# Optimization experiments

Hardware: AMD Instinct MI355X
Metric: run time of the kernel (lower is better)

## Reference

```python
import jax, jax.numpy as jnp
import numpy as np

DIM = 1024
HEADS = 16
DIM_HEAD = DIM // HEADS  # 64


def setup_inputs() -> dict:
    key = jax.random.key(0)
    k1, k2, k3 = jax.random.split(key, 3)
    x = jax.random.normal(k1, (4, 2048, DIM), dtype=jnp.float32)
    # Linear weights stored as [in, out] so y = x @ W (torch Linear uses x @ W.T; init is random either way)
    w_qkv = jax.random.normal(k2, (DIM, 3 * DIM), dtype=jnp.float32) * (DIM ** -0.5)
    w_out = jax.random.normal(k3, (DIM, DIM), dtype=jnp.float32) * (DIM ** -0.5)
    return {"x": x, "w_qkv": w_qkv, "w_out": w_out}


def reference(x, w_qkv, w_out):
    b, t, d = x.shape
    h, dh = HEADS, DIM_HEAD
    qkv = x @ w_qkv  # [b, t, 3*h*dh]
    q, k, v = jnp.split(qkv, 3, axis=-1)
    split_heads = lambda a: a.reshape(b, t, h, dh).transpose(0, 2, 1, 3)  # [b,h,t,dh]
    q, k, v = map(split_heads, (q, k, v))
    # NOTE: original scales by full model dim d, not per-head dim
    scale = d ** (-0.5)
    dots = jnp.einsum('bhie,bhje->bhij', q, k) * scale  # [b,h,t,t]
    attn = jax.nn.softmax(dots, axis=-1)
    out = jnp.einsum('bhij,bhje->bhie', attn, v)  # [b,h,t,dh]
    out = out.transpose(0, 2, 1, 3).reshape(b, t, h * dh)
    return out @ w_out
```

## Files before the change

### kernel.cpp

```cpp
#include <hip/hip_runtime.h>


typedef __bf16 bf16x8 __attribute__((ext_vector_type(8)));
typedef __bf16 bf16x4 __attribute__((ext_vector_type(4)));
typedef float f32x4 __attribute__((ext_vector_type(4)));
typedef float f32x2 __attribute__((ext_vector_type(2)));
typedef unsigned short ushort8 __attribute__((ext_vector_type(8)));

#define MFMA16(a, b, c) __builtin_amdgcn_mfma_f32_16x16x32_bf16((a), (b), (c), 0, 0, 0)

__device__ __forceinline__ unsigned short f2bf(float f) {
  unsigned int u = __float_as_uint(f);
  u = (u + 0x7FFFu + ((u >> 16) & 1u)) >> 16;
  return (unsigned short)u;
}

__device__ __forceinline__ float fast_exp2(float x) {
#if __has_builtin(__builtin_amdgcn_exp2f)
  return __builtin_amdgcn_exp2f(x);
#else
  float r;
  asm("v_exp_f32 %0, %1" : "=v"(r) : "v"(x));
  return r;
#endif
}

__device__ __forceinline__ void gload_lds16(const unsigned short* g, unsigned short* l) {
  __builtin_amdgcn_global_load_lds(
      (const __attribute__((address_space(1))) unsigned int*)g,
      (__attribute__((address_space(3))) unsigned int*)l, 16, 0, 0);
}

__global__ __launch_bounds__(256) void prep_kernel(
    const float* __restrict__ x, unsigned short* __restrict__ xb,
    const float* __restrict__ wqkv, unsigned short* __restrict__ WqkvT,
    const float* __restrict__ wout, unsigned short* __restrict__ WoutT) {
  const int bid = blockIdx.x;
  const int tid = threadIdx.x;
  if (bid < 4096) {
    int i = (bid * 256 + tid) * 8;
    float4 a = *(const float4*)&x[i];
    float4 b = *(const float4*)&x[i + 4];
    ushort8 o = {f2bf(a.x), f2bf(a.y), f2bf(a.z), f2bf(a.w),
                 f2bf(b.x), f2bf(b.y), f2bf(b.z), f2bf(b.w)};
    *(ushort8*)&xb[i] = o;
    return;
  }
  __shared__ float t[32][33];
  const float* in;
  unsigned short* out;
  int C, scale_limit, c0, r0;
  if (bid < 4096 + 3072) {
    int tj = bid - 4096;
    in = wqkv; out = WqkvT; C = 3072; scale_limit = 1024;
    c0 = (tj % 96) * 32; r0 = (tj / 96) * 32;
  } else {
    int tj = bid - 7168;
    in = wout; out = WoutT; C = 1024; scale_limit = 0;
    c0 = (tj & 31) * 32; r0 = (tj >> 5) * 32;
  }
  const float kQScale = 0.045084220027780106f;
#pragma unroll
  for (int i = 0; i < 4; ++i) {
    int e = tid + i * 256;
    int r = e >> 5, c = e & 31;
    t[r][c] = in[(size_t)(r0 + r) * C + c0 + c];
  }
  __syncthreads();
#pragma unroll
  for (int i = 0; i < 4; ++i) {
    int e = tid + i * 256;
    int r = e >> 5, c = e & 31;
    float v = t[c][r];
    if (c0 + r < scale_limit) v *= kQScale;
    out[(size_t)(c0 + r) * 1024 + r0 + c] = f2bf(v);
  }
}

template <int MODE>
__global__ __launch_bounds__(256) void gemm_bt(
    const unsigned short* __restrict__ A, const unsigned short* __restrict__ Bt,
    void* __restrict__ Cv, unsigned short* __restrict__ VT,
    int M, int N, int K) {
  __shared__ unsigned short As[128 * 32];
  __shared__ unsigned short Bs[128 * 32];
  const int tid = threadIdx.x;
  const int wave = tid >> 6, lane = tid & 63;
  const int g = lane >> 4, ln = lane & 15;
  const int wm = wave >> 1, wn = wave & 1;
  const long bm = (long)blockIdx.y * 128;
  const long bn = (long)blockIdx.x * 128;

  f32x4 acc[4][4];
#pragma unroll
  for (int i = 0; i < 4; ++i)
#pragma unroll
    for (int j = 0; j < 4; ++j) acc[i][j] = (f32x4){0.f, 0.f, 0.f, 0.f};

  const int srow = wave * 32 + (lane >> 2);
  const int scol = (lane & 3) * 8;
  const unsigned short* gA0 = A + (bm + srow) * (long)K + scol;
  const unsigned short* gA1 = gA0 + 16 * (long)K;
  const unsigned short* gB0 = Bt + (bn + srow) * (long)K + scol;
  const unsigned short* gB1 = gB0 + 16 * (long)K;
  unsigned short* lA0 = &As[wave * 1024];
  unsigned short* lA1 = &As[wave * 1024 + 512];
  unsigned short* lB0 = &Bs[wave * 1024];
  unsigned short* lB1 = &Bs[wave * 1024 + 512];

  for (int k0 = 0; k0 < K; k0 += 32) {
    __syncthreads();
    gload_lds16(gA0 + k0, lA0);
    gload_lds16(gA1 + k0, lA1);
    gload_lds16(gB0 + k0, lB0);
    gload_lds16(gB1 + k0, lB1);
    __syncthreads();

    bf16x8 af[4], bfr[4];
#pragma unroll
    for (int i = 0; i < 4; ++i) {
      af[i]  = *(const bf16x8*)&As[(wm * 64 + i * 16 + ln) * 32 + g * 8];
      bfr[i] = *(const bf16x8*)&Bs[(wn * 64 + i * 16 + ln) * 32 + g * 8];
    }
    __builtin_amdgcn_s_setprio(1);
#pragma unroll
    for (int i = 0; i < 4; ++i)
#pragma unroll
      for (int j = 0; j < 4; ++j)
        acc[i][j] = MFMA16(af[i], bfr[j], acc[i][j]);
    __builtin_amdgcn_s_setprio(0);
  }

  const long crow = bm + wm * 64, ccol = bn + wn * 64;
  if (MODE == 2 && bn >= 2048) {
#pragma unroll
    for (int i = 0; i < 4; ++i)
#pragma unroll
      for (int j = 0; j < 4; ++j) {
        int nv = (int)(ccol + j * 16 + ln) - 2048;
        int h = nv >> 6, dh = nv & 63;
        long tg = crow + i * 16 + g * 4;
        int b = (int)(tg >> 11), tl = (int)(tg & 2047);
        size_t idx = (size_t)(b * 16 + h) * 131072 + (size_t)dh * 2048 + tl;
        bf16x4 o = {(__bf16)acc[i][j][0], (__bf16)acc[i][j][1],
                    (__bf16)acc[i][j][2], (__bf16)acc[i][j][3]};
        *(bf16x4*)&VT[idx] = o;
      }
  } else {
#pragma unroll
    for (int i = 0; i < 4; ++i)
#pragma unroll
      for (int j = 0; j < 4; ++j)
#pragma unroll
        for (int r = 0; r < 4; ++r) {
          long idx = (crow + i * 16 + g * 4 + r) * (long)N + ccol + j * 16 + ln;
          if (MODE == 1)
            ((float*)Cv)[idx] = acc[i][j][r];
          else
            ((unsigned short*)Cv)[idx] = f2bf(acc[i][j][r]);
        }
  }
}

__global__ __launch_bounds__(256, 4) void attn_kernel(
    const unsigned short* __restrict__ qkv, const unsigned short* __restrict__ VT,
    unsigned short* __restrict__ attn_out) {
  __shared__ unsigned short Ks[64][72];
  __shared__ unsigned short Vs[64][72];
  __shared__ unsigned short Ps[4][2][16][72];

  const int tid = threadIdx.x;
  const int wave = tid >> 6, lane = tid & 63;
  const int g = lane >> 4, ln = lane & 15;

  const int wg = (blockIdx.x & 7) * 128 + (blockIdx.x >> 3);
  const int bh = wg >> 4, qc = wg & 15;
  const int b = bh >> 4, h = bh & 15;
  const int q0 = qc * 128;

  bf16x8 qf[2][2];
#pragma unroll
  for (int qb = 0; qb < 2; ++qb) {
    size_t base =
        (size_t)(b * 2048 + q0 + wave * 32 + qb * 16 + ln) * 3072 + h * 64 + g * 8;
    qf[qb][0] = *(const bf16x8*)&qkv[base];
    qf[qb][1] = *(const bf16x8*)&qkv[base + 32];
  }

  f32x4 oacc[2][4];
#pragma unroll
  for (int qb = 0; qb < 2; ++qb)
#pragma unroll
    for (int m = 0; m < 4; ++m) oacc[qb][m] = (f32x4){0.f, 0.f, 0.f, 0.f};
  f32x2 ls[2] = {(f32x2){0.f, 0.f}, (f32x2){0.f, 0.f}};

  const int srow = tid >> 3;
  const int sch = (tid & 7) * 8;
  const unsigned short* gK =
      qkv + (size_t)b * 2048 * 3072 + 1024 + h * 64 + (size_t)srow * 3072 + sch;
  const unsigned short* gV = VT + (size_t)bh * 131072 + (size_t)srow * 2048 + sch;

  for (int j0 = 0; j0 < 2048; j0 += 64) {
    __syncthreads();
    *(ushort8*)&Ks[srow][sch]      = *(const ushort8*)(gK + (size_t)j0 * 3072);
    *(ushort8*)&Ks[srow + 32][sch] = *(const ushort8*)(gK + (size_t)(j0 + 32) * 3072);
    *(ushort8*)&Vs[srow][sch]      = *(const ushort8*)(gV + j0);
    *(ushort8*)&Vs[srow + 32][sch] = *(const ushort8*)(gV + 32 * 2048 + j0);
    __syncthreads();

    f32x4 sacc[2][4];
#pragma unroll
    for (int qb = 0; qb < 2; ++qb)
#pragma unroll
      for (int mb = 0; mb < 4; ++mb) sacc[qb][mb] = (f32x4){0.f, 0.f, 0.f, 0.f};
    __builtin_amdgcn_s_setprio(1);
#pragma unroll
    for (int mb = 0; mb < 4; ++mb) {
      bf16x8 kf0 = *(const bf16x8*)&Ks[mb * 16 + ln][g * 8];
      bf16x8 kf1 = *(const bf16x8*)&Ks[mb * 16 + ln][32 + g * 8];
#pragma unroll
      for (int qb = 0; qb < 2; ++qb) {
        sacc[qb][mb] = MFMA16(kf0, qf[qb][0], sacc[qb][mb]);
        sacc[qb][mb] = MFMA16(kf1, qf[qb][1], sacc[qb][mb]);
      }
    }
    __builtin_amdgcn_s_setprio(0);

#pragma unroll
    for (int qb = 0; qb < 2; ++qb) {
#pragma unroll
      for (int mb = 0; mb < 4; ++mb) {
        float p0 = fast_exp2(sacc[qb][mb][0]);
        float p1 = fast_exp2(sacc[qb][mb][1]);
        float p2 = fast_exp2(sacc[qb][mb][2]);
        float p3 = fast_exp2(sacc[qb][mb][3]);
        ls[qb] += (f32x2){p0, p1} + (f32x2){p2, p3};
        bf16x4 pk = {(__bf16)p0, (__bf16)p1, (__bf16)p2, (__bf16)p3};
        *(bf16x4*)&Ps[wave][qb][ln][mb * 16 + g * 4] = pk;
      }
    }

    asm volatile("s_waitcnt lgkmcnt(0)" ::: "memory");

    bf16x8 pf[2][2];
#pragma unroll
    for (int qb = 0; qb < 2; ++qb) {
      pf[qb][0] = *(const bf16x8*)&Ps[wave][qb][ln][g * 8];
      pf[qb][1] = *(const bf16x8*)&Ps[wave][qb][ln][32 + g * 8];
    }
    __builtin_amdgcn_s_setprio(1);
#pragma unroll
    for (int mb = 0; mb < 4; ++mb) {
      bf16x8 vf0 = *(const bf16x8*)&Vs[mb * 16 + ln][g * 8];
      bf16x8 vf1 = *(const bf16x8*)&Vs[mb * 16 + ln][32 + g * 8];
#pragma unroll
      for (int qb = 0; qb < 2; ++qb) {
        oacc[qb][mb] = MFMA16(vf0, pf[qb][0], oacc[qb][mb]);
        oacc[qb][mb] = MFMA16(vf1, pf[qb][1], oacc[qb][mb]);
      }
    }
    __builtin_amdgcn_s_setprio(0);
  }

#pragma unroll
  for (int qb = 0; qb < 2; ++qb) {
    float l = ls[qb].x + ls[qb].y;
    l += __shfl_xor(l, 16);
    l += __shfl_xor(l, 32);
    float inv = 1.0f / l;
    size_t row = (size_t)(b * 2048 + q0 + wave * 32 + qb * 16 + ln) * 1024 + h * 64;
#pragma unroll
    for (int mb = 0; mb < 4; ++mb) {
      bf16x4 o = {(__bf16)(oacc[qb][mb][0] * inv), (__bf16)(oacc[qb][mb][1] * inv),
                  (__bf16)(oacc[qb][mb][2] * inv), (__bf16)(oacc[qb][mb][3] * inv)};
      *(bf16x4*)&attn_out[row + mb * 16 + g * 4] = o;
    }
  }
}

extern "C" void kernel_launch(void* const* d_in, const int* in_sizes, int n_in,
                              void* d_out, int out_size, void* d_ws, size_t ws_size,
                              hipStream_t stream) {
  (void)in_sizes; (void)n_in; (void)out_size; (void)ws_size;
  const float* x_f     = (const float*)d_in[0];
  const float* w_qkv_f = (const float*)d_in[1];
  const float* w_out_f = (const float*)d_in[2];
  float* out = (float*)d_out;

  char* ws = (char*)d_ws;
  unsigned short* qkv   = (unsigned short*)(ws);
  unsigned short* attn  = (unsigned short*)(ws + 50331648);
  unsigned short* VT    = (unsigned short*)(ws + 67108864);
  unsigned short* WqkvT = (unsigned short*)(ws + 83886080);
  unsigned short* WoutT = (unsigned short*)(ws + 90177536);
  unsigned short* xb    = (unsigned short*)(ws + 92274688);

  prep_kernel<<<8192, 256, 0, stream>>>(x_f, xb, w_qkv_f, WqkvT, w_out_f, WoutT);
  gemm_bt<2><<<dim3(24, 64), 256, 0, stream>>>(xb, WqkvT, qkv, VT, 8192, 3072, 1024);
  attn_kernel<<<1024, 256, 0, stream>>>(qkv, VT, attn);
  gemm_bt<1><<<dim3(8, 64), 256, 0, stream>>>(attn, WoutT, out, nullptr, 8192, 1024, 1024);
}
```

Baseline: 193.5 us.

## Double-buffer K/V tiles in attention with register prefetch and XOR-swizzled LDS

The attention loop now prefetches the next 64-key K and V tiles into registers while computing on the current LDS buffer, then writes them into a second LDS buffer, leaving one barrier per iteration instead of two. The LDS tiles drop their padding and use an XOR swizzle on the 8-element chunk index to avoid bank conflicts. The aim is to hide global load latency behind the MFMA and softmax work. In exchange, LDS use and register pressure go up, and launch bounds drop to 3 blocks per CU, which can lower occupancy.

```diff
diff --git a/kernel.cpp b/kernel.cpp
--- a/kernel.cpp
+++ b/kernel.cpp
@@ -162,11 +162,11 @@
   }
 }
 
-__global__ __launch_bounds__(256, 4) void attn_kernel(
+__global__ __launch_bounds__(256, 3) void attn_kernel(
     const unsigned short* __restrict__ qkv, const unsigned short* __restrict__ VT,
     unsigned short* __restrict__ attn_out) {
-  __shared__ unsigned short Ks[64][72];
-  __shared__ unsigned short Vs[64][72];
+  __shared__ unsigned short Ks[2][64][64];
+  __shared__ unsigned short Vs[2][64][64];
   __shared__ unsigned short Ps[4][2][16][72];
 
   const int tid = threadIdx.x;
@@ -195,18 +195,31 @@
   f32x2 ls[2] = {(f32x2){0.f, 0.f}, (f32x2){0.f, 0.f}};
 
   const int srow = tid >> 3;
-  const int sch = (tid & 7) * 8;
+  const int sc = tid & 7;
+  const int swc = (sc ^ (srow & 7)) * 8;
   const unsigned short* gK =
-      qkv + (size_t)b * 2048 * 3072 + 1024 + h * 64 + (size_t)srow * 3072 + sch;
-  const unsigned short* gV = VT + (size_t)bh * 131072 + (size_t)srow * 2048 + sch;
-
+      qkv + (size_t)b * 2048 * 3072 + 1024 + h * 64 + (size_t)srow * 3072 + sc * 8;
+  const unsigned short* gV = VT + (size_t)bh * 131072 + (size_t)srow * 2048 + sc * 8;
+
+  ushort8 kr0 = *(const ushort8*)(gK);
+  ushort8 kr1 = *(const ushort8*)(gK + (size_t)32 * 3072);
+  ushort8 vr0 = *(const ushort8*)(gV);
+  ushort8 vr1 = *(const ushort8*)(gV + 32 * 2048);
+  *(ushort8*)&Ks[0][srow][swc] = kr0;
+  *(ushort8*)&Ks[0][srow + 32][swc] = kr1;
+  *(ushort8*)&Vs[0][srow][swc] = vr0;
+  *(ushort8*)&Vs[0][srow + 32][swc] = vr1;
+  __syncthreads();
+
+  int cur = 0;
   for (int j0 = 0; j0 < 2048; j0 += 64) {
-    __syncthreads();
-    *(ushort8*)&Ks[srow][sch]      = *(const ushort8*)(gK + (size_t)j0 * 3072);
-    *(ushort8*)&Ks[srow + 32][sch] = *(const ushort8*)(gK + (size_t)(j0 + 32) * 3072);
-    *(ushort8*)&Vs[srow][sch]      = *(const ushort8*)(gV + j0);
-    *(ushort8*)&Vs[srow + 32][sch] = *(const ushort8*)(gV + 32 * 2048 + j0);
-    __syncthreads();
+    const bool more = (j0 + 64) < 2048;
+    if (more) {
+      kr0 = *(const ushort8*)(gK + (size_t)(j0 + 64) * 3072);
+      kr1 = *(const ushort8*)(gK + (size_t)(j0 + 96) * 3072);
+      vr0 = *(const ushort8*)(gV + (j0 + 64));
+      vr1 = *(const ushort8*)(gV + 32 * 2048 + (j0 + 64));
+    }
 
     f32x4 sacc[2][4];
 #pragma unroll
@@ -216,8 +229,8 @@
     __builtin_amdgcn_s_setprio(1);
 #pragma unroll
     for (int mb = 0; mb < 4; ++mb) {
-      bf16x8 kf0 = *(const bf16x8*)&Ks[mb * 16 + ln][g * 8];
-      bf16x8 kf1 = *(const bf16x8*)&Ks[mb * 16 + ln][32 + g * 8];
+      bf16x8 kf0 = *(const bf16x8*)&Ks[cur][mb * 16 + ln][(g ^ (ln & 7)) * 8];
+      bf16x8 kf1 = *(const bf16x8*)&Ks[cur][mb * 16 + ln][((4 + g) ^ (ln & 7)) * 8];
 #pragma unroll
       for (int qb = 0; qb < 2; ++qb) {
         sacc[qb][mb] = MFMA16(kf0, qf[qb][0], sacc[qb][mb]);
@@ -251,8 +264,8 @@
     __builtin_amdgcn_s_setprio(1);
 #pragma unroll
     for (int mb = 0; mb < 4; ++mb) {
-      bf16x8 vf0 = *(const bf16x8*)&Vs[mb * 16 + ln][g * 8];
-      bf16x8 vf1 = *(const bf16x8*)&Vs[mb * 16 + ln][32 + g * 8];
+      bf16x8 vf0 = *(const bf16x8*)&Vs[cur][mb * 16 + ln][(g ^ (ln & 7)) * 8];
+      bf16x8 vf1 = *(const bf16x8*)&Vs[cur][mb * 16 + ln][((4 + g) ^ (ln & 7)) * 8];
 #pragma unroll
       for (int qb = 0; qb < 2; ++qb) {
         oacc[qb][mb] = MFMA16(vf0, pf[qb][0], oacc[qb][mb]);
@@ -260,6 +273,15 @@
       }
     }
     __builtin_amdgcn_s_setprio(0);
+
+    if (more) {
+      *(ushort8*)&Ks[cur ^ 1][srow][swc] = kr0;
+      *(ushort8*)&Ks[cur ^ 1][srow + 32][swc] = kr1;
+      *(ushort8*)&Vs[cur ^ 1][srow][swc] = vr0;
+      *(ushort8*)&Vs[cur ^ 1][srow + 32][swc] = vr1;
+    }
+    __syncthreads();
+    cur ^= 1;
   }
 
 #pragma unroll
```

Measured after the change: 200.8 us. +3.8%, slower.

## Switch attention to 32x32 MFMA with register P exchange and swizzled LDS

Applied to the files above, without the earlier changes.

Rewrites the attention inner loop to use 32x32x16 bf16 MFMA tiles instead of 16x16x32. The probability tile is passed from the QK^T accumulator layout into the PV operand layout through cross-lane shuffles instead of a round trip through shared memory. K and V tiles in shared memory switch from padded rows to an XOR-swizzled layout. The aim is to cut LDS traffic, the wait on the P store, and MFMA issue count, at the cost of a more intricate register mapping and more shuffle instructions.

```diff
diff --git a/kernel.cpp b/kernel.cpp
--- a/kernel.cpp
+++ b/kernel.cpp
@@ -3,11 +3,14 @@
 
 typedef __bf16 bf16x8 __attribute__((ext_vector_type(8)));
 typedef __bf16 bf16x4 __attribute__((ext_vector_type(4)));
+typedef __bf16 bf16x2 __attribute__((ext_vector_type(2)));
 typedef float f32x4 __attribute__((ext_vector_type(4)));
 typedef float f32x2 __attribute__((ext_vector_type(2)));
+typedef float f32x16 __attribute__((ext_vector_type(16)));
 typedef unsigned short ushort8 __attribute__((ext_vector_type(8)));
 
 #define MFMA16(a, b, c) __builtin_amdgcn_mfma_f32_16x16x32_bf16((a), (b), (c), 0, 0, 0)
+#define MFMA32(a, b, c) __builtin_amdgcn_mfma_f32_32x32x16_bf16((a), (b), (c), 0, 0, 0)
 
 __device__ __forceinline__ unsigned short f2bf(float f) {
   unsigned int u = __float_as_uint(f);
@@ -165,117 +168,111 @@
 __global__ __launch_bounds__(256, 4) void attn_kernel(
     const unsigned short* __restrict__ qkv, const unsigned short* __restrict__ VT,
     unsigned short* __restrict__ attn_out) {
-  __shared__ unsigned short Ks[64][72];
-  __shared__ unsigned short Vs[64][72];
-  __shared__ unsigned short Ps[4][2][16][72];
+  __shared__ unsigned short Ks[64][64];
+  __shared__ unsigned short Vs[64][64];
 
   const int tid = threadIdx.x;
   const int wave = tid >> 6, lane = tid & 63;
-  const int g = lane >> 4, ln = lane & 15;
+  const int l31 = lane & 31, hb = lane >> 5;
 
   const int wg = (blockIdx.x & 7) * 128 + (blockIdx.x >> 3);
   const int bh = wg >> 4, qc = wg & 15;
-  const int b = bh >> 4, h = bh & 15;
-  const int q0 = qc * 128;
-
-  bf16x8 qf[2][2];
-#pragma unroll
-  for (int qb = 0; qb < 2; ++qb) {
-    size_t base =
-        (size_t)(b * 2048 + q0 + wave * 32 + qb * 16 + ln) * 3072 + h * 64 + g * 8;
-    qf[qb][0] = *(const bf16x8*)&qkv[base];
-    qf[qb][1] = *(const bf16x8*)&qkv[base + 32];
-  }
-
-  f32x4 oacc[2][4];
-#pragma unroll
-  for (int qb = 0; qb < 2; ++qb)
-#pragma unroll
-    for (int m = 0; m < 4; ++m) oacc[qb][m] = (f32x4){0.f, 0.f, 0.f, 0.f};
-  f32x2 ls[2] = {(f32x2){0.f, 0.f}, (f32x2){0.f, 0.f}};
+  const int b = bh >> 4, head = bh & 15;
+  const int q0 = qc * 128 + wave * 32;
+
+  bf16x8 qf[4];
+  {
+    size_t base = (size_t)(b * 2048 + q0 + l31) * 3072 + head * 64 + 8 * hb;
+    qf[0] = *(const bf16x8*)&qkv[base];
+    qf[1] = *(const bf16x8*)&qkv[base + 16];
+    qf[2] = *(const bf16x8*)&qkv[base + 32];
+    qf[3] = *(const bf16x8*)&qkv[base + 48];
+  }
+
+  f32x16 oacc[2];
+#pragma unroll
+  for (int i = 0; i < 16; ++i) { oacc[0][i] = 0.f; oacc[1][i] = 0.f; }
+  f32x2 ls = {0.f, 0.f};
 
   const int srow = tid >> 3;
-  const int sch = (tid & 7) * 8;
+  const int sc = tid & 7;
+  const int swc = (sc ^ (srow & 7)) * 8;
   const unsigned short* gK =
-      qkv + (size_t)b * 2048 * 3072 + 1024 + h * 64 + (size_t)srow * 3072 + sch;
-  const unsigned short* gV = VT + (size_t)bh * 131072 + (size_t)srow * 2048 + sch;
+      qkv + (size_t)b * 2048 * 3072 + 1024 + head * 64 + (size_t)srow * 3072 + sc * 8;
+  const unsigned short* gV = VT + (size_t)bh * 131072 + (size_t)srow * 2048 + sc * 8;
+
+  const int myx = l31 & 7;
 
   for (int j0 = 0; j0 < 2048; j0 += 64) {
     __syncthreads();
-    *(ushort8*)&Ks[srow][sch]      = *(const ushort8*)(gK + (size_t)j0 * 3072);
-    *(ushort8*)&Ks[srow + 32][sch] = *(const ushort8*)(gK + (size_t)(j0 + 32) * 3072);
-    *(ushort8*)&Vs[srow][sch]      = *(const ushort8*)(gV + j0);
-    *(ushort8*)&Vs[srow + 32][sch] = *(const ushort8*)(gV + 32 * 2048 + j0);
-    __syncthreads();
-
-    f32x4 sacc[2][4];
-#pragma unroll
-    for (int qb = 0; qb < 2; ++qb)
-#pragma unroll
-      for (int mb = 0; mb < 4; ++mb) sacc[qb][mb] = (f32x4){0.f, 0.f, 0.f, 0.f};
-    __builtin_amdgcn_s_setprio(1);
-#pragma unroll
-    for (int mb = 0; mb < 4; ++mb) {
-      bf16x8 kf0 = *(const bf16x8*)&Ks[mb * 16 + ln][g * 8];
-      bf16x8 kf1 = *(const bf16x8*)&Ks[mb * 16 + ln][32 + g * 8];
-#pragma unroll
-      for (int qb = 0; qb < 2; ++qb) {
-        sacc[qb][mb] = MFMA16(kf0, qf[qb][0], sacc[qb][mb]);
-        sacc[qb][mb] = MFMA16(kf1, qf[qb][1], sacc[qb][mb]);
-      }
+    *(ushort8*)&Ks[srow][swc]      = *(const ushort8*)(gK + (size_t)j0 * 3072);
+    *(ushort8*)&Ks[srow + 32][swc] = *(const ushort8*)(gK + (size_t)(j0 + 32) * 3072);
+    *(ushort8*)&Vs[srow][swc]      = *(const ushort8*)(gV + j0);
+    *(ushort8*)&Vs[srow + 32][swc] = *(const ushort8*)(gV + 32 * 2048 + j0);
+    __syncthreads();
+
+#pragma unroll
+    for (int kt = 0; kt < 2; ++kt) {
+      f32x16 sa;
+#pragma unroll
+      for (int i = 0; i < 16; ++i) sa[i] = 0.f;
+      __builtin_amdgcn_s_setprio(1);
+#pragma unroll
+      for (int t = 0; t < 4; ++t) {
+        bf16x8 kf = *(const bf16x8*)&Ks[kt * 32 + l31][((2 * t + hb) ^ myx) * 8];
+        sa = MFMA32(kf, qf[t], sa);
+      }
+      __builtin_amdgcn_s_setprio(0);
+
+      unsigned int pkw[8], opk[8];
+#pragma unroll
+      for (int j = 0; j < 8; ++j) {
+        float p0 = fast_exp2(sa[2 * j]);
+        float p1 = fast_exp2(sa[2 * j + 1]);
+        ls += (f32x2){p0, p1};
+        bf16x2 pv = {(__bf16)p0, (__bf16)p1};
+        pkw[j] = __builtin_bit_cast(unsigned int, pv);
+      }
+#pragma unroll
+      for (int j = 0; j < 8; ++j) opk[j] = (unsigned int)__shfl_xor((int)pkw[j], 32);
+
+      const bool H = (hb != 0);
+      union { unsigned int u[4]; bf16x8 v; } pf0, pf1;
+      pf0.u[0] = H ? opk[2] : pkw[0];
+      pf0.u[1] = H ? opk[3] : pkw[1];
+      pf0.u[2] = H ? pkw[2] : opk[0];
+      pf0.u[3] = H ? pkw[3] : opk[1];
+      pf1.u[0] = H ? opk[6] : pkw[4];
+      pf1.u[1] = H ? opk[7] : pkw[5];
+      pf1.u[2] = H ? pkw[6] : opk[4];
+      pf1.u[3] = H ? pkw[7] : opk[5];
+
+      __builtin_amdgcn_s_setprio(1);
+#pragma unroll
+      for (int mt = 0; mt < 2; ++mt) {
+        bf16x8 vf0 = *(const bf16x8*)&Vs[mt * 32 + l31][((4 * kt + hb) ^ myx) * 8];
+        bf16x8 vf1 = *(const bf16x8*)&Vs[mt * 32 + l31][((4 * kt + 2 + hb) ^ myx) * 8];
+        oacc[mt] = MFMA32(vf0, pf0.v, oacc[mt]);
+        oacc[mt] = MFMA32(vf1, pf1.v, oacc[mt]);
+      }
+      __builtin_amdgcn_s_setprio(0);
     }
-    __builtin_amdgcn_s_setprio(0);
-
-#pragma unroll
-    for (int qb = 0; qb < 2; ++qb) {
-#pragma unroll
-      for (int mb = 0; mb < 4; ++mb) {
-        float p0 = fast_exp2(sacc[qb][mb][0]);
-        float p1 = fast_exp2(sacc[qb][mb][1]);
-        float p2 = fast_exp2(sacc[qb][mb][2]);
-        float p3 = fast_exp2(sacc[qb][mb][3]);
-        ls[qb] += (f32x2){p0, p1} + (f32x2){p2, p3};
-        bf16x4 pk = {(__bf16)p0, (__bf16)p1, (__bf16)p2, (__bf16)p3};
-        *(bf16x4*)&Ps[wave][qb][ln][mb * 16 + g * 4] = pk;
-      }
+  }
+
+  float l = ls.x + ls.y;
+  l += __shfl_xor(l, 32);
+  float inv = 1.0f / l;
+  size_t row = (size_t)(b * 2048 + q0 + l31) * 1024 + head * 64;
+#pragma unroll
+  for (int mt = 0; mt < 2; ++mt)
+#pragma unroll
+    for (int rq = 0; rq < 4; ++rq) {
+      bf16x4 o = {(__bf16)(oacc[mt][4 * rq + 0] * inv),
+                  (__bf16)(oacc[mt][4 * rq + 1] * inv),
+                  (__bf16)(oacc[mt][4 * rq + 2] * inv),
+                  (__bf16)(oacc[mt][4 * rq + 3] * inv)};
+      *(bf16x4*)&attn_out[row + mt * 32 + 8 * rq + 4 * hb] = o;
     }
-
-    asm volatile("s_waitcnt lgkmcnt(0)" ::: "memory");
-
-    bf16x8 pf[2][2];
-#pragma unroll
-    for (int qb = 0; qb < 2; ++qb) {
-      pf[qb][0] = *(const bf16x8*)&Ps[wave][qb][ln][g * 8];
-      pf[qb][1] = *(const bf16x8*)&Ps[wave][qb][ln][32 + g * 8];
-    }
-    __builtin_amdgcn_s_setprio(1);
-#pragma unroll
-    for (int mb = 0; mb < 4; ++mb) {
-      bf16x8 vf0 = *(const bf16x8*)&Vs[mb * 16 + ln][g * 8];
-      bf16x8 vf1 = *(const bf16x8*)&Vs[mb * 16 + ln][32 + g * 8];
-#pragma unroll
-      for (int qb = 0; qb < 2; ++qb) {
-        oacc[qb][mb] = MFMA16(vf0, pf[qb][0], oacc[qb][mb]);
-        oacc[qb][mb] = MFMA16(vf1, pf[qb][1], oacc[qb][mb]);
-      }
-    }
-    __builtin_amdgcn_s_setprio(0);
-  }
-
-#pragma unroll
-  for (int qb = 0; qb < 2; ++qb) {
-    float l = ls[qb].x + ls[qb].y;
-    l += __shfl_xor(l, 16);
-    l += __shfl_xor(l, 32);
-    float inv = 1.0f / l;
-    size_t row = (size_t)(b * 2048 + q0 + wave * 32 + qb * 16 + ln) * 1024 + h * 64;
-#pragma unroll
-    for (int mb = 0; mb < 4; ++mb) {
-      bf16x4 o = {(__bf16)(oacc[qb][mb][0] * inv), (__bf16)(oacc[qb][mb][1] * inv),
-                  (__bf16)(oacc[qb][mb][2] * inv), (__bf16)(oacc[qb][mb][3] * inv)};
-      *(bf16x4*)&attn_out[row + mb * 16 + g * 4] = o;
-    }
-  }
 }
 
 extern "C" void kernel_launch(void* const* d_in, const int* in_sizes, int n_in,
```

Measured after the change: 196.9 us. About the same (+1.8%).
